# Kernel optimization log

Hardware: AMD Instinct MI355X
Metric: run time of the kernel (lower is better)

The kernel has to match this reference:

```python
import jax, jax.numpy as jnp
import numpy as np
from jax import lax

B, T, D, H = 256, 128, 512, 512  # batch, time, input feat, n_hidden


def _lstm_dir(x, W, U, b, reverse):
    """Single-direction Keras-convention LSTM scan.
    x: [B,T,D]; W: [D,4H]; U: [H,4H]; b: [4H]. Gate order i,f,c,o.
    Returns (hs [B,T,H] in original time order, h_final [B,H])."""
    xw = jnp.einsum('btd,dg->btg', x, W) + b          # precompute input projections
    xs = jnp.swapaxes(xw, 0, 1)                        # [T,B,4H]
    h0 = jnp.zeros((x.shape[0], U.shape[0]), x.dtype)
    c0 = jnp.zeros_like(h0)

    def step(carry, xt):
        h, c = carry
        z = xt + h @ U                                 # [B,4H]
        i, f, g, o = jnp.split(z, 4, axis=-1)
        i = jax.nn.sigmoid(i)
        f = jax.nn.sigmoid(f)
        g = jnp.tanh(g)
        o = jax.nn.sigmoid(o)
        c = f * c + i * g
        h = o * jnp.tanh(c)
        return (h, c), h

    (hT, cT), hs = lax.scan(step, (h0, c0), xs, reverse=reverse)
    return jnp.swapaxes(hs, 0, 1), hT


def setup_inputs() -> dict:
    key = jax.random.key(0)
    kx, k1, k2, k3, k4 = jax.random.split(key, 5)
    s_in = 1.0 / np.sqrt(D)
    s_h = 1.0 / np.sqrt(H)
    x = jax.random.normal(kx, (B, T, D), dtype=jnp.float32)
    W_f = jax.random.normal(k1, (D, 4 * H), dtype=jnp.float32) * s_in
    U_f = jax.random.normal(k2, (H, 4 * H), dtype=jnp.float32) * s_h
    b_f = jnp.concatenate([jnp.zeros(H), jnp.ones(H), jnp.zeros(2 * H)]).astype(jnp.float32)  # unit_forget_bias
    W_b = jax.random.normal(k3, (D, 4 * H), dtype=jnp.float32) * s_in
    U_b = jax.random.normal(k4, (H, 4 * H), dtype=jnp.float32) * s_h
    b_b = b_f
    return {"x": x, "W_f": W_f, "U_f": U_f, "b_f": b_f, "W_b": W_b, "U_b": U_b, "b_b": b_b}


def reference(x, W_f, U_f, b_f, W_b, U_b, b_b):
    # forward direction
    hs_f, hT_f = _lstm_dir(x, W_f, U_f, b_f, reverse=False)
    # backward direction: processes t=T-1..0; outputs re-aligned to original order
    hs_b, hT_b = _lstm_dir(x, W_b, U_b, b_b, reverse=True)
    word_emb = jnp.concatenate([hs_f, hs_b], axis=-1)   # [B,T,2H]
    sent_emb = jnp.concatenate([hT_f, hT_b], axis=-1)   # [B,2H]
    return word_emb, sent_emb
```

## Files before the change

kernel.cpp:

```cpp
#include <hip/hip_runtime.h>
#include <stdint.h>

#define BB 256
#define TT 128
#define DD 512
#define HH 512
#define G4 2048

typedef short bf16x8 __attribute__((ext_vector_type(8)));
typedef float f32x4  __attribute__((ext_vector_type(4)));
typedef int   i32x4  __attribute__((ext_vector_type(4)));

__device__ __forceinline__ unsigned short f2bf(float f){
  union { float f; unsigned u; } v; v.f = f;
  unsigned u = v.u;
  unsigned r = (u + 0x7FFFu + ((u >> 16) & 1u)) >> 16;
  return (unsigned short)r;
}
__device__ __forceinline__ float bf2f(unsigned short s){
  union { unsigned u; float f; } v; v.u = ((unsigned)s) << 16;
  return v.f;
}
__device__ __forceinline__ float sigf(float x){
  return __builtin_amdgcn_rcpf(1.0f + __expf(-x));
}
__device__ __forceinline__ float tanhfast(float x){
  return 1.0f - 2.0f*__builtin_amdgcn_rcpf(1.0f + __expf(2.0f*x));
}

__global__ void prep_x_k(const float* __restrict__ x, unsigned short* __restrict__ xtr){
  const int n4 = BB*TT*(DD/4);
  for (int i = blockIdx.x*blockDim.x + threadIdx.x; i < n4; i += gridDim.x*blockDim.x){
    int d4 = i & (DD/4 - 1);
    int b  = (i / (DD/4)) & (BB-1);
    int t  = i / ((DD/4)*BB);
    float4 v = *(const float4*)(x + (((size_t)b*TT + t)*DD + (size_t)d4*4));
    ushort4 o;
    o.x = f2bf(v.x); o.y = f2bf(v.y); o.z = f2bf(v.z); o.w = f2bf(v.w);
    *(ushort4*)(xtr + (((size_t)t*BB + b)*DD + (size_t)d4*4)) = o;
  }
}

__global__ void prep_wu_k(const float* __restrict__ Wf, const float* __restrict__ Uf,
                          const float* __restrict__ Wb, const float* __restrict__ Ub,
                          unsigned short* __restrict__ wupk){
  const int tot = 2*2*32*16*4*64*8;
  for (int i = blockIdx.x*blockDim.x + threadIdx.x; i < tot; i += gridDim.x*blockDim.x){
    int e    = i & 7;
    int lane = (i >> 3) & 63;
    int gf   = (i >> 9) & 3;
    int ks   = (i >> 11) & 15;
    int hb   = (i >> 15) & 31;
    int d    = (i >> 20) & 1;
    int arr  = (i >> 21) & 1;
    int jl = lane & 15, q = lane >> 4;
    int n = gf*HH + hb*16 + jl;
    int k = ks*32 + q*8 + e;
    const float* src = arr ? (d ? Ub : Uf) : (d ? Wb : Wf);
    wupk[i] = f2bf(src[(size_t)k*G4 + n]);
  }
}

__global__ void prep_bias_k(const float* __restrict__ bf_, const float* __restrict__ bb_,
                            float* __restrict__ bias_pk){
  int i = blockIdx.x*blockDim.x + threadIdx.x;
  if (i < 2*32*4*16){
    int jl = i & 15;
    int gf = (i >> 4) & 3;
    int hb = (i >> 6) & 31;
    int d  = i >> 11;
    const float* src = d ? bb_ : bf_;
    bias_pk[i] = src[gf*HH + hb*16 + jl];
  }
}

__global__ __launch_bounds__(384, 1)
void lstm_fused_k(const unsigned short* __restrict__ xtr,
                  const unsigned short* __restrict__ wupk,
                  const float* __restrict__ bias_pk,
                  unsigned short* hgrp,
                  int* flags, int* xcdcnt,
                  float* __restrict__ out)
{
  __shared__ __align__(1024) unsigned short Wl[32768];
  __shared__ __align__(1024) unsigned short Ul[32768];
  __shared__ __align__(1024) unsigned short ringB[2][4096];
  __shared__ int xseq[2];
  __shared__ int cseq[4];
  __shared__ int go;
  __shared__ int done;
  __shared__ int shId[4];

  const int tid  = threadIdx.x;
  const int lane = tid & 63;
  const int w    = tid >> 6;
  const int jl   = lane & 15, q = lane >> 4;

  if (tid == 0){
    unsigned xcd;
    asm volatile("s_getreg_b32 %0, hwreg(HW_REG_XCC_ID)" : "=s"(xcd));
    int x = (int)(xcd & 7);
    int rank = __hip_atomic_fetch_add(&xcdcnt[x], 1, __ATOMIC_RELAXED, __HIP_MEMORY_SCOPE_AGENT);
    __hip_atomic_fetch_add(&xcdcnt[8], 1, __ATOMIC_RELEASE, __HIP_MEMORY_SCOPE_AGENT);
    while (__hip_atomic_load(&xcdcnt[8], __ATOMIC_ACQUIRE, __HIP_MEMORY_SCOPE_AGENT) < 256)
      __builtin_amdgcn_s_sleep(2);
    int n[8];
    #pragma unroll
    for (int i = 0; i < 8; ++i)
      n[i] = __hip_atomic_load(&xcdcnt[i], __ATOMIC_RELAXED, __HIP_MEMORY_SCOPE_AGENT);
    int gg = 0, hh = 0;
    if (rank < 32){ gg = x; hh = rank; }
    else {
      int k = rank - 32;
      for (int i = 0; i < x; ++i) if (n[i] > 32) k += n[i] - 32;
      for (int i = 0; i < 8; ++i){
        int def = 32 - n[i];
        if (def > 0){
          if (k < def){ gg = i; hh = n[i] + k; break; }
          k -= def;
        }
      }
    }
    shId[0] = gg; shId[1] = hh; shId[2] = (n[gg] >= 32) ? 1 : 0;
    go = 0; done = 0;
  }
  if (tid < 2) xseq[tid] = 0;
  if (tid < 4) cseq[tid] = 0;
  __syncthreads();
  const int g    = shId[0];
  const int hb   = shId[1];
  const int pure = shId[2];
  const int d    = g >> 2;
  const int mq   = g & 3;
  const int m0   = mq * 64;

  const unsigned short* wsrc = wupk + ((size_t)(0*2 + d)*32 + hb)*32768;
  const unsigned short* usrc = wupk + ((size_t)(1*2 + d)*32 + hb)*32768;
  for (int u = tid; u < 4096; u += 384){
    __builtin_amdgcn_global_load_lds(
      (const __attribute__((address_space(1))) void*)(wsrc + (size_t)u*8),
      (__attribute__((address_space(3))) void*)(Wl + u*8), 16, 0, 0);
    __builtin_amdgcn_global_load_lds(
      (const __attribute__((address_space(1))) void*)(usrc + (size_t)u*8),
      (__attribute__((address_space(3))) void*)(Ul + u*8), 16, 0, 0);
  }
  __syncthreads();

  unsigned short* hgbase = hgrp + (size_t)g*65536;

  if (w >= 4){
    const int w2 = w - 4;
    float biasv[4];
    #pragma unroll
    for (int gf = 0; gf < 4; ++gf)
      biasv[gf] = bias_pk[((d*32 + hb)*4 + gf)*16 + jl];

    for (int s = 0; s < TT; ++s){
      const int t = d ? (TT-1-s) : s;
      if (s >= 2){
        while (__hip_atomic_load(&cseq[2*w2],   __ATOMIC_ACQUIRE, __HIP_MEMORY_SCOPE_WORKGROUP) < s-1 ||
               __hip_atomic_load(&cseq[2*w2+1], __ATOMIC_ACQUIRE, __HIP_MEMORY_SCOPE_WORKGROUP) < s-1) {}
      }
      const unsigned short* xb = xtr + ((size_t)t*BB + m0 + w2*32)*DD;
      bf16x8 xa[2][16];
      #pragma unroll
      for (int ks = 0; ks < 16; ++ks)
        #pragma unroll
        for (int am = 0; am < 2; ++am)
          xa[am][ks] = *(const bf16x8*)(xb + (size_t)(am*16 + jl)*DD + ks*32 + q*8);

      f32x4 acc[2][4];
      #pragma unroll
      for (int am = 0; am < 2; ++am)
        #pragma unroll
        for (int gf = 0; gf < 4; ++gf){
          float bv = biasv[gf];
          acc[am][gf] = (f32x4){bv, bv, bv, bv};
        }

      #pragma unroll
      for (int ks = 0; ks < 16; ++ks){
        #pragma unroll
        for (int gf = 0; gf < 4; ++gf){
          bf16x8 b = *(const bf16x8*)(Wl + ((ks*4 + gf)*64 + lane)*8);
          #pragma unroll
          for (int am = 0; am < 2; ++am)
            acc[am][gf] = __builtin_amdgcn_mfma_f32_16x16x32_bf16(xa[am][ks], b, acc[am][gf], 0, 0, 0);
        }
      }

      const int slot = s & 1;
      #pragma unroll
      for (int am = 0; am < 2; ++am)
        #pragma unroll
        for (int gf = 0; gf < 4; ++gf)
          #pragma unroll
          for (int rr = 0; rr < 4; ++rr)
            ringB[slot][(w2*32 + am*16 + q*4 + rr)*64 + gf*16 + jl] = f2bf(acc[am][gf][rr]);
      __hip_atomic_store(&xseq[w2], s+1, __ATOMIC_RELEASE, __HIP_MEMORY_SCOPE_WORKGROUP);
    }
  } else {
    float cst[4] = {0.f, 0.f, 0.f, 0.f};
    int* myflags = flags + g*64;

    for (int s = 0; s < TT; ++s){
      const int t   = d ? (TT-1-s) : s;
      const int par = s & 1;

      while (__hip_atomic_load(&xseq[w >> 1], __ATOMIC_ACQUIRE, __HIP_MEMORY_SCOPE_WORKGROUP) < s+1) {}
      float zx[4][4];
      #pragma unroll
      for (int gf = 0; gf < 4; ++gf)
        #pragma unroll
        for (int rr = 0; rr < 4; ++rr)
          zx[gf][rr] = bf2f(ringB[par][(w*16 + q*4 + rr)*64 + gf*16 + jl]);
      __hip_atomic_store(&cseq[w], s+1, __ATOMIC_RELEASE, __HIP_MEMORY_SCOPE_WORKGROUP);

      if (s > 0){
        if (w == 0){
          for (;;){
            int v = (lane < 32)
              ? __hip_atomic_load(myflags + lane, __ATOMIC_RELAXED, __HIP_MEMORY_SCOPE_AGENT)
              : s;
            if (__all(v >= s)) break;
            __builtin_amdgcn_s_sleep(1);
          }
          __hip_atomic_store(&go, s, __ATOMIC_RELEASE, __HIP_MEMORY_SCOPE_WORKGROUP);
        } else {
          while (__hip_atomic_load(&go, __ATOMIC_ACQUIRE, __HIP_MEMORY_SCOPE_WORKGROUP) < s) {}
        }
      }
      asm volatile("" ::: "memory");

      const char* hgp = (const char*)hgbase + (size_t)par*65536;
      union Q { i32x4 i; unsigned long long u[2]; bf16x8 v; } ha[16];
      if (pure){
        #pragma unroll
        for (int ks = 0; ks < 16; ++ks){
          const void* p = (const void*)
              (hgp + (((ks*2 + (q>>1))*64 + w*16 + jl)*32 + (q&1)*16));
          asm volatile("global_load_dwordx4 %0, %1, off sc0"
                       : "=v"(ha[ks].i) : "v"(p));
        }
        asm volatile("s_waitcnt vmcnt(0)" ::: "memory");
        __builtin_amdgcn_sched_barrier(0);
      } else {
        #pragma unroll
        for (int ks = 0; ks < 16; ++ks){
          const unsigned long long* p = (const unsigned long long*)
              (hgp + (((ks*2 + (q>>1))*64 + w*16 + jl)*32 + (q&1)*16));
          ha[ks].u[0] = __hip_atomic_load(p,     __ATOMIC_RELAXED, __HIP_MEMORY_SCOPE_AGENT);
          ha[ks].u[1] = __hip_atomic_load(p + 1, __ATOMIC_RELAXED, __HIP_MEMORY_SCOPE_AGENT);
        }
      }

      f32x4 acc[4];
      #pragma unroll
      for (int gf = 0; gf < 4; ++gf) acc[gf] = (f32x4){0.f,0.f,0.f,0.f};

      #pragma unroll
      for (int ks = 0; ks < 16; ++ks){
        #pragma unroll
        for (int gf = 0; gf < 4; ++gf){
          bf16x8 b = *(const bf16x8*)(Ul + ((ks*4 + gf)*64 + lane)*8);
          acc[gf] = __builtin_amdgcn_mfma_f32_16x16x32_bf16(ha[ks].v, b, acc[gf], 0, 0, 0);
        }
      }

      unsigned short* hc = hgbase + (size_t)(((s+1)&1)*32 + hb)*1024;
      float hov[4];
      #pragma unroll
      for (int rr = 0; rr < 4; ++rr){
        float zi = acc[0][rr] + zx[0][rr];
        float zf = acc[1][rr] + zx[1][rr];
        float zg = acc[2][rr] + zx[2][rr];
        float zo = acc[3][rr] + zx[3][rr];
        float i_ = sigf(zi);
        float f_ = sigf(zf);
        float g_ = tanhfast(zg);
        float o_ = sigf(zo);
        float c  = f_*cst[rr] + i_*g_;
        cst[rr] = c;
        float h = o_*tanhfast(c);
        hov[rr] = h;

        int row64 = w*16 + q*4 + rr;
        unsigned short h16 = f2bf(h);
        int other = __shfl_xor((int)h16, 1);
        if (!(jl & 1)){
          unsigned int pack = (unsigned int)h16 | (((unsigned int)other & 0xFFFFu) << 16);
          unsigned int* dst = (unsigned int*)(hc + row64*16 + (jl & ~1));
          if (pure) *dst = pack;
          else __hip_atomic_store(dst, pack, __ATOMIC_RELAXED, __HIP_MEMORY_SCOPE_AGENT);
        }
      }

      asm volatile("s_waitcnt vmcnt(0)" ::: "memory");
      if (lane == 0)
        __hip_atomic_fetch_add(&done, 1, __ATOMIC_ACQ_REL, __HIP_MEMORY_SCOPE_WORKGROUP);
      if (w == 0){
        while (__hip_atomic_load(&done, __ATOMIC_ACQUIRE, __HIP_MEMORY_SCOPE_WORKGROUP) < 4*(s+1)) {}
        if (lane == 0)
          __hip_atomic_store(myflags + hb, s + 1, __ATOMIC_RELAXED, __HIP_MEMORY_SCOPE_AGENT);
      }

      #pragma unroll
      for (int rr = 0; rr < 4; ++rr){
        int b_ = m0 + w*16 + q*4 + rr;
        out[((size_t)b_*TT + t)*(2*HH) + (size_t)d*HH + hb*16 + jl] = hov[rr];
      }
    }
  }
}

__global__ void final_k(float* __restrict__ out){
  int i = blockIdx.x*blockDim.x + threadIdx.x;
  if (i < BB*2*HH){
    int b = i >> 10;
    int n = i & 1023;
    int t = (n < HH) ? (TT-1) : 0;
    out[(size_t)BB*TT*2*HH + i] = out[((size_t)b*TT + t)*2*HH + n];
  }
}

extern "C" void kernel_launch(void* const* d_in, const int* in_sizes, int n_in,
                              void* d_out, int out_size, void* d_ws, size_t ws_size,
                              hipStream_t stream)
{
  const float* x   = (const float*)d_in[0];
  const float* Wf  = (const float*)d_in[1];
  const float* Uf  = (const float*)d_in[2];
  const float* bf_ = (const float*)d_in[3];
  const float* Wb  = (const float*)d_in[4];
  const float* Ub  = (const float*)d_in[5];
  const float* bb_ = (const float*)d_in[6];
  float* out = (float*)d_out;

  char* ws = (char*)d_ws;
  unsigned short* xtr  = (unsigned short*)(ws);
  unsigned short* wupk = (unsigned short*)(ws + 33554432);
  float* bias_pk       = (float*)(ws + 41943040);
  unsigned short* hgrp = (unsigned short*)(ws + 41959424);
  int* flags           = (int*)(ws + 44056576);
  int* xcdcnt          = (int*)(ws + 44058624);

  hipMemsetAsync(hgrp, 0, 2097152, stream);
  hipMemsetAsync(flags, 0, 2048, stream);
  hipMemsetAsync(xcdcnt, 0, 64, stream);

  prep_x_k   <<<2048, 256, 0, stream>>>(x, xtr);
  prep_wu_k  <<<4096, 256, 0, stream>>>(Wf, Uf, Wb, Ub, wupk);
  prep_bias_k<<<16,   256, 0, stream>>>(bf_, bb_, bias_pk);

  lstm_fused_k<<<256, 384, 0, stream>>>(xtr, wupk, bias_pk, hgrp, flags, xcdcnt, out);

  final_k<<<1024, 256, 0, stream>>>(out);
}
```

Baseline: 580.4 us.

## Use per-wave global step flags instead of block-level done/go barrier

Each of the four recurrent waves now publishes its own step flag to global memory, and every wave polls all 128 flags of its group directly. This removes the intra-block done counter and go broadcast, taking one serialized handoff out of each timestep's critical path. The ring buffer is also XOR-swizzled to cut LDS bank conflicts, and the LDS spin waits now sleep between polls. The costs are twice the flag traffic and every wave polling global memory instead of only one.

```diff
diff --git a/kernel.cpp b/kernel.cpp
--- a/kernel.cpp
+++ b/kernel.cpp
@@ -87,8 +87,6 @@
   __shared__ __align__(1024) unsigned short ringB[2][4096];
   __shared__ int xseq[2];
   __shared__ int cseq[4];
-  __shared__ int go;
-  __shared__ int done;
   __shared__ int shId[4];
 
   const int tid  = threadIdx.x;
@@ -122,7 +120,6 @@
       }
     }
     shId[0] = gg; shId[1] = hh; shId[2] = (n[gg] >= 32) ? 1 : 0;
-    go = 0; done = 0;
   }
   if (tid < 2) xseq[tid] = 0;
   if (tid < 4) cseq[tid] = 0;
@@ -159,7 +156,8 @@
       const int t = d ? (TT-1-s) : s;
       if (s >= 2){
         while (__hip_atomic_load(&cseq[2*w2],   __ATOMIC_ACQUIRE, __HIP_MEMORY_SCOPE_WORKGROUP) < s-1 ||
-               __hip_atomic_load(&cseq[2*w2+1], __ATOMIC_ACQUIRE, __HIP_MEMORY_SCOPE_WORKGROUP) < s-1) {}
+               __hip_atomic_load(&cseq[2*w2+1], __ATOMIC_ACQUIRE, __HIP_MEMORY_SCOPE_WORKGROUP) < s-1)
+          __builtin_amdgcn_s_sleep(1);
       }
       const unsigned short* xb = xtr + ((size_t)t*BB + m0 + w2*32)*DD;
       bf16x8 xa[2][16];
@@ -196,38 +194,34 @@
         for (int gf = 0; gf < 4; ++gf)
           #pragma unroll
           for (int rr = 0; rr < 4; ++rr)
-            ringB[slot][(w2*32 + am*16 + q*4 + rr)*64 + gf*16 + jl] = f2bf(acc[am][gf][rr]);
+            ringB[slot][(w2*32 + am*16 + q*4 + rr)*64 + ((gf*16 + jl) ^ (q << 2))] =
+                f2bf(acc[am][gf][rr]);
       __hip_atomic_store(&xseq[w2], s+1, __ATOMIC_RELEASE, __HIP_MEMORY_SCOPE_WORKGROUP);
     }
   } else {
     float cst[4] = {0.f, 0.f, 0.f, 0.f};
-    int* myflags = flags + g*64;
+    int* myflags = flags + g*128;
 
     for (int s = 0; s < TT; ++s){
       const int t   = d ? (TT-1-s) : s;
       const int par = s & 1;
 
-      while (__hip_atomic_load(&xseq[w >> 1], __ATOMIC_ACQUIRE, __HIP_MEMORY_SCOPE_WORKGROUP) < s+1) {}
+      while (__hip_atomic_load(&xseq[w >> 1], __ATOMIC_ACQUIRE, __HIP_MEMORY_SCOPE_WORKGROUP) < s+1)
+        __builtin_amdgcn_s_sleep(1);
       float zx[4][4];
       #pragma unroll
       for (int gf = 0; gf < 4; ++gf)
         #pragma unroll
         for (int rr = 0; rr < 4; ++rr)
-          zx[gf][rr] = bf2f(ringB[par][(w*16 + q*4 + rr)*64 + gf*16 + jl]);
+          zx[gf][rr] = bf2f(ringB[par][(w*16 + q*4 + rr)*64 + ((gf*16 + jl) ^ (q << 2))]);
       __hip_atomic_store(&cseq[w], s+1, __ATOMIC_RELEASE, __HIP_MEMORY_SCOPE_WORKGROUP);
 
       if (s > 0){
-        if (w == 0){
-          for (;;){
-            int v = (lane < 32)
-              ? __hip_atomic_load(myflags + lane, __ATOMIC_RELAXED, __HIP_MEMORY_SCOPE_AGENT)
-              : s;
-            if (__all(v >= s)) break;
-            __builtin_amdgcn_s_sleep(1);
-          }
-          __hip_atomic_store(&go, s, __ATOMIC_RELEASE, __HIP_MEMORY_SCOPE_WORKGROUP);
-        } else {
-          while (__hip_atomic_load(&go, __ATOMIC_ACQUIRE, __HIP_MEMORY_SCOPE_WORKGROUP) < s) {}
+        for (;;){
+          int v0 = __hip_atomic_load(myflags + lane,      __ATOMIC_RELAXED, __HIP_MEMORY_SCOPE_AGENT);
+          int v1 = __hip_atomic_load(myflags + 64 + lane, __ATOMIC_RELAXED, __HIP_MEMORY_SCOPE_AGENT);
+          if (__all(v0 >= s && v1 >= s)) break;
+          __builtin_amdgcn_s_sleep(1);
         }
       }
       asm volatile("" ::: "memory");
@@ -297,12 +291,7 @@
 
       asm volatile("s_waitcnt vmcnt(0)" ::: "memory");
       if (lane == 0)
-        __hip_atomic_fetch_add(&done, 1, __ATOMIC_ACQ_REL, __HIP_MEMORY_SCOPE_WORKGROUP);
-      if (w == 0){
-        while (__hip_atomic_load(&done, __ATOMIC_ACQUIRE, __HIP_MEMORY_SCOPE_WORKGROUP) < 4*(s+1)) {}
-        if (lane == 0)
-          __hip_atomic_store(myflags + hb, s + 1, __ATOMIC_RELAXED, __HIP_MEMORY_SCOPE_AGENT);
-      }
+        __hip_atomic_store(myflags + hb*4 + w, s + 1, __ATOMIC_RELAXED, __HIP_MEMORY_SCOPE_AGENT);
 
       #pragma unroll
       for (int rr = 0; rr < 4; ++rr){
@@ -342,10 +331,10 @@
   float* bias_pk       = (float*)(ws + 41943040);
   unsigned short* hgrp = (unsigned short*)(ws + 41959424);
   int* flags           = (int*)(ws + 44056576);
-  int* xcdcnt          = (int*)(ws + 44058624);
+  int* xcdcnt          = (int*)(ws + 44060672);
 
   hipMemsetAsync(hgrp, 0, 2097152, stream);
-  hipMemsetAsync(flags, 0, 2048, stream);
+  hipMemsetAsync(flags, 0, 4096, stream);
   hipMemsetAsync(xcdcnt, 0, 64, stream);
 
   prep_x_k   <<<2048, 256, 0, stream>>>(x, xtr);
```

Result: slower. 871.8 us (+50.2%).
